# Kernel tuning notes

Hardware: AMD Instinct MI355X
Metric: run time of the kernel (lower is better)

Reference implementation:

```python
import jax, jax.numpy as jnp
import numpy as np

N_POI = 100000
N_USER = 20000
NNZ = 300000
EMB = 256


def spmm(rows, cols, vals, dense, n_rows):
    """COO sparse [n_rows, n_cols] @ dense [n_cols, D] -> [n_rows, D]."""
    # gather edge-source features, scale by edge value, scatter-add into rows
    msg = vals[:, None] * dense[cols]            # [nnz, D]
    return jax.ops.segment_sum(msg, rows, num_segments=n_rows)


def setup_inputs() -> dict:
    key = jax.random.key(0)
    ks = jax.random.split(key, 7)
    return {
        "pois_embs": jax.random.normal(ks[0], (N_POI, EMB), dtype=jnp.float32),
        "up_rows": jax.random.randint(ks[1], (NNZ,), 0, N_USER, dtype=jnp.int32),
        "up_cols": jax.random.randint(ks[2], (NNZ,), 0, N_POI, dtype=jnp.int32),
        "up_vals": jax.random.uniform(ks[3], (NNZ,), dtype=jnp.float32),
        "pu_rows": jax.random.randint(ks[4], (NNZ,), 0, N_POI, dtype=jnp.int32),
        "pu_cols": jax.random.randint(ks[5], (NNZ,), 0, N_USER, dtype=jnp.int32),
        "pu_vals": jax.random.uniform(ks[6], (NNZ,), dtype=jnp.float32),
    }


def reference(pois_embs, up_rows, up_cols, up_vals, pu_rows, pu_cols, pu_vals):
    # hop 1: user hyperedge aggregation  msg_poi_agg = HG_up @ pois_embs
    msg_poi_agg = spmm(up_rows, up_cols, up_vals, pois_embs, N_USER)   # [N_USER, EMB]
    # hop 2: propagate back to POIs      propag = HG_pu @ msg_poi_agg
    propag_pois_embs = spmm(pu_rows, pu_cols, pu_vals, msg_poi_agg, N_POI)  # [N_POI, EMB]
    return propag_pois_embs
```

## Files before the change

### kernel.cpp

```cpp
#include <hip/hip_runtime.h>
#include <hip/hip_bf16.h>

#define N_POI  100000
#define N_USER 20000
#define NNZ    300000
#define EMB    256


__global__ void zero_ints(int* __restrict__ p, int n) {
    int i = blockIdx.x * blockDim.x + threadIdx.x;
    int s = gridDim.x * blockDim.x;
    for (; i < n; i += s) p[i] = 0;
}

__global__ void count_kernel(const int* __restrict__ rows, int* __restrict__ cnt, int nnz) {
    int i = blockIdx.x * blockDim.x + threadIdx.x;
    int s = gridDim.x * blockDim.x;
    for (; i < nnz; i += s) atomicAdd(&cnt[rows[i]], 1);
}

__global__ void alloc_kernel(const int* __restrict__ cnt, int* __restrict__ start,
                             int* __restrict__ cursor, int n) {
    int i = blockIdx.x * blockDim.x + threadIdx.x;
    int s = gridDim.x * blockDim.x;
    for (; i < n; i += s) start[i] = atomicAdd(cursor, cnt[i]);
}

__global__ void fill_kernel(const int* __restrict__ rows, const int* __restrict__ start,
                            int* __restrict__ fill, int* __restrict__ eidx, int nnz) {
    int i = blockIdx.x * blockDim.x + threadIdx.x;
    int s = gridDim.x * blockDim.x;
    for (; i < nnz; i += s) {
        int r = rows[i];
        int p = atomicAdd(&fill[r], 1);
        eidx[start[r] + p] = i;
    }
}


__global__ void gather_kernel(const int* __restrict__ start, const int* __restrict__ cnt,
                              const int* __restrict__ eidx, const int* __restrict__ cols,
                              const float* __restrict__ vals, const float* __restrict__ dense,
                              float* __restrict__ out, int n_rows) {
    int gid  = blockIdx.x * blockDim.x + threadIdx.x;
    int row  = gid >> 6;
    int lane = gid & 63;
    if (row >= n_rows) return;

    int s = start[row];
    int c = cnt[row];

    float4 acc = make_float4(0.f, 0.f, 0.f, 0.f);
    for (int k = 0; k < c; ++k) {
        int   e   = eidx[s + k];
        int   col = cols[e];
        float v   = vals[e];
        const float4 m = *(reinterpret_cast<const float4*>(dense + (size_t)col * EMB) + lane);
        acc.x += v * m.x;
        acc.y += v * m.y;
        acc.z += v * m.z;
        acc.w += v * m.w;
    }
    *(reinterpret_cast<float4*>(out + (size_t)row * EMB) + lane) = acc;
}


extern "C" void kernel_launch(void* const* d_in, const int* in_sizes, int n_in,
                              void* d_out, int out_size, void* d_ws, size_t ws_size,
                              hipStream_t stream) {
    const float* pois_embs = (const float*)d_in[0];
    const int*   up_rows   = (const int*)d_in[1];
    const int*   up_cols   = (const int*)d_in[2];
    const float* up_vals   = (const float*)d_in[3];
    const int*   pu_rows   = (const int*)d_in[4];
    const int*   pu_cols   = (const int*)d_in[5];
    const float* pu_vals   = (const float*)d_in[6];

    float* out = (float*)d_out;

    char* ws = (char*)d_ws;
    size_t off = 0;
    auto take = [&](size_t bytes) { char* p = ws + off; off += (bytes + 15) & ~size_t(15); return p; };

    float* msg      = (float*)take((size_t)N_USER * EMB * sizeof(float));
    int* ctrl       = (int*)take((size_t)(3 * N_USER + 3 * N_POI + 2) * sizeof(int));
    int* up_cnt     = ctrl;
    int* up_start   = up_cnt + N_USER;
    int* up_fill    = up_start + N_USER;
    int* pu_cnt     = up_fill + N_USER;
    int* pu_start   = pu_cnt + N_POI;
    int* pu_fill    = pu_start + N_POI;
    int* cursors    = pu_fill + N_POI;
    int* up_eidx    = (int*)take((size_t)NNZ * sizeof(int));
    int* pu_eidx    = (int*)take((size_t)NNZ * sizeof(int));

    const int ctrl_n = 3 * N_USER + 3 * N_POI + 2;

    zero_ints<<<512, 256, 0, stream>>>(ctrl, ctrl_n);

    count_kernel<<<1024, 256, 0, stream>>>(up_rows, up_cnt, NNZ);
    count_kernel<<<1024, 256, 0, stream>>>(pu_rows, pu_cnt, NNZ);

    alloc_kernel<<<256, 256, 0, stream>>>(up_cnt, up_start, &cursors[0], N_USER);
    alloc_kernel<<<512, 256, 0, stream>>>(pu_cnt, pu_start, &cursors[1], N_POI);

    fill_kernel<<<1024, 256, 0, stream>>>(up_rows, up_start, up_fill, up_eidx, NNZ);
    fill_kernel<<<1024, 256, 0, stream>>>(pu_rows, pu_start, pu_fill, pu_eidx, NNZ);

    {
        int blocks = (N_USER * 64 + 255) / 256;
        gather_kernel<<<blocks, 256, 0, stream>>>(
            up_start, up_cnt, up_eidx, up_cols, up_vals, pois_embs, msg, N_USER);
    }

    {
        int blocks = (N_POI * 64 + 255) / 256;
        gather_kernel<<<blocks, 256, 0, stream>>>(
            pu_start, pu_cnt, pu_eidx, pu_cols, pu_vals, msg, out, N_POI);
    }
}
```

Before: 392.7 us.

## Store permuted cols/vals in CSR order, fuse setup kernels, unroll gather by four

The fill step now writes column indices and values directly into row-sorted arrays, with each row padded to a multiple of four, instead of an edge-index permutation. The gather can then load four cols and vals at once as aligned int4/float4 and issue four independent dense-row loads per iteration, removing the double indirection through eidx. The up and pu count, alloc and fill kernels are merged to cut the launch count. The cost is larger padded workspace arrays and branches inside the merged kernels.

Measured after the change: 342.9 us. 1.15x faster.

```diff
diff --git a/kernel.cpp b/kernel.cpp
--- a/kernel.cpp
+++ b/kernel.cpp
@@ -13,35 +13,63 @@
     for (; i < n; i += s) p[i] = 0;
 }
 
-__global__ void count_kernel(const int* __restrict__ rows, int* __restrict__ cnt, int nnz) {
+__global__ void count_both(const int* __restrict__ up_rows, int* __restrict__ up_cnt,
+                           const int* __restrict__ pu_rows, int* __restrict__ pu_cnt) {
     int i = blockIdx.x * blockDim.x + threadIdx.x;
     int s = gridDim.x * blockDim.x;
-    for (; i < nnz; i += s) atomicAdd(&cnt[rows[i]], 1);
+    for (; i < 2 * NNZ; i += s) {
+        if (i < NNZ) atomicAdd(&up_cnt[up_rows[i]], 1);
+        else         atomicAdd(&pu_cnt[pu_rows[i - NNZ]], 1);
+    }
 }
 
-__global__ void alloc_kernel(const int* __restrict__ cnt, int* __restrict__ start,
-                             int* __restrict__ cursor, int n) {
+__global__ void alloc_both(const int* __restrict__ up_cnt, int* __restrict__ up_start,
+                           const int* __restrict__ pu_cnt, int* __restrict__ pu_start,
+                           int* __restrict__ cursors) {
     int i = blockIdx.x * blockDim.x + threadIdx.x;
     int s = gridDim.x * blockDim.x;
-    for (; i < n; i += s) start[i] = atomicAdd(cursor, cnt[i]);
+    for (; i < N_USER + N_POI; i += s) {
+        if (i < N_USER) up_start[i] = atomicAdd(&cursors[0], (up_cnt[i] + 3) & ~3);
+        else {
+            int r = i - N_USER;
+            pu_start[r] = atomicAdd(&cursors[1], (pu_cnt[r] + 3) & ~3);
+        }
+    }
 }
 
-__global__ void fill_kernel(const int* __restrict__ rows, const int* __restrict__ start,
-                            int* __restrict__ fill, int* __restrict__ eidx, int nnz) {
+__global__ void fill_both(const int* __restrict__ up_rows, const int* __restrict__ up_cols,
+                          const float* __restrict__ up_vals, const int* __restrict__ up_start,
+                          int* __restrict__ up_fill, int* __restrict__ up_cols_r,
+                          float* __restrict__ up_vals_r,
+                          const int* __restrict__ pu_rows, const int* __restrict__ pu_cols,
+                          const float* __restrict__ pu_vals, const int* __restrict__ pu_start,
+                          int* __restrict__ pu_fill, int* __restrict__ pu_cols_r,
+                          float* __restrict__ pu_vals_r) {
     int i = blockIdx.x * blockDim.x + threadIdx.x;
     int s = gridDim.x * blockDim.x;
-    for (; i < nnz; i += s) {
-        int r = rows[i];
-        int p = atomicAdd(&fill[r], 1);
-        eidx[start[r] + p] = i;
+    for (; i < 2 * NNZ; i += s) {
+        if (i < NNZ) {
+            int r = up_rows[i];
+            int p = atomicAdd(&up_fill[r], 1);
+            int d = up_start[r] + p;
+            up_cols_r[d] = up_cols[i];
+            up_vals_r[d] = up_vals[i];
+        } else {
+            int e = i - NNZ;
+            int r = pu_rows[e];
+            int p = atomicAdd(&pu_fill[r], 1);
+            int d = pu_start[r] + p;
+            pu_cols_r[d] = pu_cols[e];
+            pu_vals_r[d] = pu_vals[e];
+        }
     }
 }
 
 
 __global__ void gather_kernel(const int* __restrict__ start, const int* __restrict__ cnt,
-                              const int* __restrict__ eidx, const int* __restrict__ cols,
-                              const float* __restrict__ vals, const float* __restrict__ dense,
-                              float* __restrict__ out, int n_rows) {
+                              const int* __restrict__ cols_r, const float* __restrict__ vals_r,
+                              const float* __restrict__ dense, float* __restrict__ out,
+                              int n_rows) {
     int gid  = blockIdx.x * blockDim.x + threadIdx.x;
     int row  = gid >> 6;
     int lane = gid & 63;
@@ -51,10 +79,22 @@
     int c = cnt[row];
 
     float4 acc = make_float4(0.f, 0.f, 0.f, 0.f);
-    for (int k = 0; k < c; ++k) {
-        int   e   = eidx[s + k];
-        int   col = cols[e];
-        float v   = vals[e];
+    int k = 0;
+    for (; k + 4 <= c; k += 4) {
+        int4   c4 = *reinterpret_cast<const int4*>(cols_r + s + k);
+        float4 v4 = *reinterpret_cast<const float4*>(vals_r + s + k);
+        const float4 m0 = *(reinterpret_cast<const float4*>(dense + (size_t)c4.x * EMB) + lane);
+        const float4 m1 = *(reinterpret_cast<const float4*>(dense + (size_t)c4.y * EMB) + lane);
+        const float4 m2 = *(reinterpret_cast<const float4*>(dense + (size_t)c4.z * EMB) + lane);
+        const float4 m3 = *(reinterpret_cast<const float4*>(dense + (size_t)c4.w * EMB) + lane);
+        acc.x += v4.x * m0.x + v4.y * m1.x + v4.z * m2.x + v4.w * m3.x;
+        acc.y += v4.x * m0.y + v4.y * m1.y + v4.z * m2.y + v4.w * m3.y;
+        acc.z += v4.x * m0.z + v4.y * m1.z + v4.z * m2.z + v4.w * m3.z;
+        acc.w += v4.x * m0.w + v4.y * m1.w + v4.z * m2.w + v4.w * m3.w;
+    }
+    for (; k < c; ++k) {
+        int   col = cols_r[s + k];
+        float v   = vals_r[s + k];
         const float4 m = *(reinterpret_cast<const float4*>(dense + (size_t)col * EMB) + lane);
         acc.x += v * m.x;
         acc.y += v * m.y;
@@ -82,40 +122,35 @@
     size_t off = 0;
     auto take = [&](size_t bytes) { char* p = ws + off; off += (bytes + 15) & ~size_t(15); return p; };
 
-    float* msg      = (float*)take((size_t)N_USER * EMB * sizeof(float));
-    int* ctrl       = (int*)take((size_t)(3 * N_USER + 3 * N_POI + 2) * sizeof(int));
-    int* up_cnt     = ctrl;
-    int* up_start   = up_cnt + N_USER;
-    int* up_fill    = up_start + N_USER;
-    int* pu_cnt     = up_fill + N_USER;
-    int* pu_start   = pu_cnt + N_POI;
-    int* pu_fill    = pu_start + N_POI;
-    int* cursors    = pu_fill + N_POI;
-    int* up_eidx    = (int*)take((size_t)NNZ * sizeof(int));
-    int* pu_eidx    = (int*)take((size_t)NNZ * sizeof(int));
+    float* msg    = (float*)take((size_t)N_USER * EMB * sizeof(float));
+    int*   ctrl   = (int*)take((size_t)(3 * N_USER + 3 * N_POI + 2) * sizeof(int));
+    int* up_cnt   = ctrl;
+    int* up_start = up_cnt + N_USER;
+    int* up_fill  = up_start + N_USER;
+    int* pu_cnt   = up_fill + N_USER;
+    int* pu_start = pu_cnt + N_POI;
+    int* pu_fill  = pu_start + N_POI;
+    int* cursors  = pu_fill + N_POI;
+
+    const int up_cap = NNZ + 4 * N_USER;
+    const int pu_cap = NNZ + 4 * N_POI;
+    int*   up_cols_r = (int*)  take((size_t)up_cap * sizeof(int));
+    float* up_vals_r = (float*)take((size_t)up_cap * sizeof(float));
+    int*   pu_cols_r = (int*)  take((size_t)pu_cap * sizeof(int));
+    float* pu_vals_r = (float*)take((size_t)pu_cap * sizeof(float));
 
     const int ctrl_n = 3 * N_USER + 3 * N_POI + 2;
 
     zero_ints<<<512, 256, 0, stream>>>(ctrl, ctrl_n);
+    count_both<<<1024, 256, 0, stream>>>(up_rows, up_cnt, pu_rows, pu_cnt);
+    alloc_both<<<512, 256, 0, stream>>>(up_cnt, up_start, pu_cnt, pu_start, cursors);
+    fill_both<<<1024, 256, 0, stream>>>(
+        up_rows, up_cols, up_vals, up_start, up_fill, up_cols_r, up_vals_r,
+        pu_rows, pu_cols, pu_vals, pu_start, pu_fill, pu_cols_r, pu_vals_r);
 
-    count_kernel<<<1024, 256, 0, stream>>>(up_rows, up_cnt, NNZ);
-    count_kernel<<<1024, 256, 0, stream>>>(pu_rows, pu_cnt, NNZ);
+    gather_kernel<<<(N_USER * 64) / 256, 256, 0, stream>>>(
+        up_start, up_cnt, up_cols_r, up_vals_r, pois_embs, msg, N_USER);
 
-    alloc_kernel<<<256, 256, 0, stream>>>(up_cnt, up_start, &cursors[0], N_USER);
-    alloc_kernel<<<512, 256, 0, stream>>>(pu_cnt, pu_start, &cursors[1], N_POI);
-
-    fill_kernel<<<1024, 256, 0, stream>>>(up_rows, up_start, up_fill, up_eidx, NNZ);
-    fill_kernel<<<1024, 256, 0, stream>>>(pu_rows, pu_start, pu_fill, pu_eidx, NNZ);
-
-    {
-        int blocks = (N_USER * 64 + 255) / 256;
-        gather_kernel<<<blocks, 256, 0, stream>>>(
-            up_start, up_cnt, up_eidx, up_cols, up_vals, pois_embs, msg, N_USER);
-    }
-
-    {
-        int blocks = (N_POI * 64 + 255) / 256;
-        gather_kernel<<<blocks, 256, 0, stream>>>(
-            pu_start, pu_cnt, pu_eidx, pu_cols, pu_vals, msg, out, N_POI);
-    }
+    gather_kernel<<<(N_POI * 64) / 256, 256, 0, stream>>>(
+        pu_start, pu_cnt, pu_cols_r, pu_vals_r, msg, out, N_POI);
 }
```
